# Kernel tuning notes

Hardware: AMD Instinct MI355X
Metric: run time of the kernel (lower is better)

## Reference

```python
import jax, jax.numpy as jnp
import numpy as np

MARGIN = 0.5
EPS = 1e-8  # torch CosineSimilarity eps


def setup_inputs() -> dict:
    key = jax.random.key(0)
    k1, k2 = jax.random.split(key)
    line_end_embeddings = jax.random.normal(k1, (4096, 32, 256), dtype=jnp.float32)
    rhyme_scheme = jax.random.randint(k2, (4096, 32), 0, 4, dtype=jnp.int32)
    return {"line_end_embeddings": line_end_embeddings, "rhyme_scheme": rhyme_scheme}


def reference(line_end_embeddings, rhyme_scheme):
    b, n, d = line_end_embeddings.shape
    # cosine similarity with torch-style eps clamping on norms
    norms = jnp.maximum(jnp.linalg.norm(line_end_embeddings, axis=-1, keepdims=True), EPS)
    unit = line_end_embeddings / norms                       # [b, n, d]
    sims = jnp.einsum("bid,bjd->bij", unit, unit)            # [b, n, n]
    same = rhyme_scheme[:, :, None] == rhyme_scheme[:, None, :]  # [b, n, n]
    per_pair = jnp.where(same, 1.0 - sims, jax.nn.relu(sims - MARGIN))
    # only pairs i < j (strict upper triangle)
    upper = jnp.triu(jnp.ones((n, n), dtype=bool), k=1)
    total = jnp.sum(per_pair * upper[None, :, :])
    count = b * (n * (n - 1) // 2)
    return total / max(count, 1)
```

## Files before the change

kernel.cpp:

```cpp
#include <hip/hip_runtime.h>
#include <hip/hip_bf16.h>


typedef short bf16x8 __attribute__((ext_vector_type(8)));
typedef float f32x4  __attribute__((ext_vector_type(4)));

#define MARGIN 0.5f
#define EPS_NORM 1e-8f
#define NPAIR_INV (1.0f / 2031616.0f)

static __device__ __forceinline__ short f2bf(float f) {
    unsigned u = __float_as_uint(f);
    u += 0x7fffu + ((u >> 16) & 1u);
    return (short)(u >> 16);
}

__global__ __launch_bounds__(256) void rhyme_loss_kernel(
    const float* __restrict__ emb,
    const int*   __restrict__ sch,
    float*       __restrict__ out)
{
    __shared__ float s_diag[4][32];
    __shared__ float s_inv[4][32];
    __shared__ int   s_sch[4][32];

    const int tid  = threadIdx.x;
    const int w    = tid >> 6;
    const int lane = tid & 63;
    const int b    = blockIdx.x * 4 + w;

    const int q = lane >> 4;
    const int c = lane & 15;

    const float* base0 = emb + (size_t)b * 8192 + (size_t)c * 256 + q * 8;
    const float* base1 = base0 + 16 * 256;

    f32x4 acc00 = {0.f, 0.f, 0.f, 0.f};
    f32x4 acc01 = {0.f, 0.f, 0.f, 0.f};
    f32x4 acc11 = {0.f, 0.f, 0.f, 0.f};

    #pragma unroll
    for (int kc = 0; kc < 256; kc += 32) {
        const float4* p0 = (const float4*)(base0 + kc);
        const float4* p1 = (const float4*)(base1 + kc);
        float4 a0 = p0[0], a1 = p0[1];
        float4 b0 = p1[0], b1 = p1[1];

        bf16x8 f0, f1;
        f0[0] = f2bf(a0.x); f0[1] = f2bf(a0.y); f0[2] = f2bf(a0.z); f0[3] = f2bf(a0.w);
        f0[4] = f2bf(a1.x); f0[5] = f2bf(a1.y); f0[6] = f2bf(a1.z); f0[7] = f2bf(a1.w);
        f1[0] = f2bf(b0.x); f1[1] = f2bf(b0.y); f1[2] = f2bf(b0.z); f1[3] = f2bf(b0.w);
        f1[4] = f2bf(b1.x); f1[5] = f2bf(b1.y); f1[6] = f2bf(b1.z); f1[7] = f2bf(b1.w);

        acc00 = __builtin_amdgcn_mfma_f32_16x16x32_bf16(f0, f0, acc00, 0, 0, 0);
        acc01 = __builtin_amdgcn_mfma_f32_16x16x32_bf16(f0, f1, acc01, 0, 0, 0);
        acc11 = __builtin_amdgcn_mfma_f32_16x16x32_bf16(f1, f1, acc11, 0, 0, 0);
    }

    const int dreg = c - 4 * q;
    if (dreg >= 0 && dreg < 4) {
        s_diag[w][c]      = acc00[dreg];
        s_diag[w][16 + c] = acc11[dreg];
    }
    __syncthreads();

    if (lane < 32) {
        float d = s_diag[w][lane];
        s_inv[w][lane] = 1.0f / fmaxf(sqrtf(d), EPS_NORM);
        s_sch[w][lane] = sch[b * 32 + lane];
    }
    __syncthreads();

    const float invj0 = s_inv[w][c];
    const float invj1 = s_inv[w][16 + c];
    const int   sj0   = s_sch[w][c];
    const int   sj1   = s_sch[w][16 + c];

    float sum = 0.0f;
    #pragma unroll
    for (int r = 0; r < 4; ++r) {
        const int   i0    = q * 4 + r;
        const float inv_i = s_inv[w][i0];
        const int   si    = s_sch[w][i0];

        {
            float sim = acc01[r] * inv_i * invj1;
            sum += (si == sj1) ? (1.0f - sim) : fmaxf(sim - MARGIN, 0.0f);
        }
        if (i0 < c) {
            float sim = acc00[r] * inv_i * invj0;
            sum += (si == sj0) ? (1.0f - sim) : fmaxf(sim - MARGIN, 0.0f);
            float sim2 = acc11[r] * s_inv[w][16 + i0] * invj1;
            sum += (s_sch[w][16 + i0] == sj1) ? (1.0f - sim2)
                                              : fmaxf(sim2 - MARGIN, 0.0f);
        }
    }

    #pragma unroll
    for (int off = 32; off > 0; off >>= 1)
        sum += __shfl_down(sum, off, 64);

    if (lane == 0)
        atomicAdd(out, sum * NPAIR_INV);
}

extern "C" void kernel_launch(void* const* d_in, const int* in_sizes, int n_in,
                              void* d_out, int out_size, void* d_ws, size_t ws_size,
                              hipStream_t stream) {
    const float* emb = (const float*)d_in[0];
    const int*   sch = (const int*)d_in[1];
    float*       out = (float*)d_out;

    hipMemsetAsync(out, 0, sizeof(float), stream);
    rhyme_loss_kernel<<<dim3(4096 / 4), dim3(256), 0, stream>>>(emb, sch, out);
}
```

Baseline: 232.9 us.

## Stage embedding rows into LDS via direct global-to-LDS loads, one batch per block

Each batch element's 32x256 fp32 rows are now copied into padded shared memory with global_load_lds, so the global reads are fully coalesced 16-byte-per-lane loads instead of strided per-row float4 loads. The MFMA operands are then read from LDS, with a row stride of 260 to avoid bank conflicts. The launch becomes one 64-thread block per batch, which gives 4x more blocks and one atomic per block. The waitcnt immediate is hard-coded, and each block uses about 33KB of LDS, which limits how many blocks can be resident per CU.

```diff
diff --git a/kernel.cpp b/kernel.cpp
--- a/kernel.cpp
+++ b/kernel.cpp
@@ -1,5 +1,6 @@
 #include <hip/hip_runtime.h>
 #include <hip/hip_bf16.h>
+#include <stdint.h>
 
 
 typedef short bf16x8 __attribute__((ext_vector_type(8)));
@@ -8,6 +9,10 @@
 #define MARGIN 0.5f
 #define EPS_NORM 1e-8f
 #define NPAIR_INV (1.0f / 2031616.0f)
+#define ROW_STRIDE 260
+
+typedef const __attribute__((address_space(1))) void GVOID;
+typedef __attribute__((address_space(3))) void LVOID;
 
 static __device__ __forceinline__ short f2bf(float f) {
     unsigned u = __float_as_uint(f);
@@ -15,25 +20,40 @@
     return (short)(u >> 16);
 }
 
-__global__ __launch_bounds__(256) void rhyme_loss_kernel(
+__global__ __launch_bounds__(64) void rhyme_loss_kernel(
     const float* __restrict__ emb,
     const int*   __restrict__ sch,
     float*       __restrict__ out)
 {
-    __shared__ float s_diag[4][32];
-    __shared__ float s_inv[4][32];
-    __shared__ int   s_sch[4][32];
+    __shared__ float s_rows[32 * ROW_STRIDE];
+    __shared__ float s_inv[32];
+    __shared__ float s_diag[32];
+    __shared__ int   s_sch[32];
 
-    const int tid  = threadIdx.x;
-    const int w    = tid >> 6;
-    const int lane = tid & 63;
-    const int b    = blockIdx.x * 4 + w;
+    const int lane = threadIdx.x;
+    const int b    = blockIdx.x;
 
     const int q = lane >> 4;
     const int c = lane & 15;
 
-    const float* base0 = emb + (size_t)b * 8192 + (size_t)c * 256 + q * 8;
-    const float* base1 = base0 + 16 * 256;
+    const float* gbase = emb + (size_t)b * 8192 + (size_t)lane * 4;
+    #pragma unroll
+    for (int r = 0; r < 32; ++r) {
+        __builtin_amdgcn_global_load_lds(
+            (GVOID*)(gbase + r * 256),
+            (LVOID*)(&s_rows[r * ROW_STRIDE]),
+            16, 0, 0);
+    }
+
+    int mysch = (lane < 32) ? sch[(size_t)b * 32 + lane] : 0;
+
+    __builtin_amdgcn_s_waitcnt(0x0f70);
+    __syncthreads();
+
+    if (lane < 32) s_sch[lane] = mysch;
+
+    const float* r0 = s_rows + (size_t)c * ROW_STRIDE + q * 8;
+    const float* r1 = s_rows + (size_t)(16 + c) * ROW_STRIDE + q * 8;
 
     f32x4 acc00 = {0.f, 0.f, 0.f, 0.f};
     f32x4 acc01 = {0.f, 0.f, 0.f, 0.f};
@@ -41,8 +61,8 @@
 
     #pragma unroll
     for (int kc = 0; kc < 256; kc += 32) {
-        const float4* p0 = (const float4*)(base0 + kc);
-        const float4* p1 = (const float4*)(base1 + kc);
+        const float4* p0 = (const float4*)(r0 + kc);
+        const float4* p1 = (const float4*)(r1 + kc);
         float4 a0 = p0[0], a1 = p0[1];
         float4 b0 = p1[0], b1 = p1[1];
 
@@ -59,29 +79,28 @@
 
     const int dreg = c - 4 * q;
     if (dreg >= 0 && dreg < 4) {
-        s_diag[w][c]      = acc00[dreg];
-        s_diag[w][16 + c] = acc11[dreg];
+        s_diag[c]      = acc00[dreg];
+        s_diag[16 + c] = acc11[dreg];
     }
     __syncthreads();
 
     if (lane < 32) {
-        float d = s_diag[w][lane];
-        s_inv[w][lane] = 1.0f / fmaxf(sqrtf(d), EPS_NORM);
-        s_sch[w][lane] = sch[b * 32 + lane];
+        float d = s_diag[lane];
+        s_inv[lane] = 1.0f / fmaxf(sqrtf(d), EPS_NORM);
     }
     __syncthreads();
 
-    const float invj0 = s_inv[w][c];
-    const float invj1 = s_inv[w][16 + c];
-    const int   sj0   = s_sch[w][c];
-    const int   sj1   = s_sch[w][16 + c];
+    const float invj0 = s_inv[c];
+    const float invj1 = s_inv[16 + c];
+    const int   sj0   = s_sch[c];
+    const int   sj1   = s_sch[16 + c];
 
     float sum = 0.0f;
     #pragma unroll
     for (int r = 0; r < 4; ++r) {
         const int   i0    = q * 4 + r;
-        const float inv_i = s_inv[w][i0];
-        const int   si    = s_sch[w][i0];
+        const float inv_i = s_inv[i0];
+        const int   si    = s_sch[i0];
 
         {
             float sim = acc01[r] * inv_i * invj1;
@@ -90,9 +109,9 @@
         if (i0 < c) {
             float sim = acc00[r] * inv_i * invj0;
             sum += (si == sj0) ? (1.0f - sim) : fmaxf(sim - MARGIN, 0.0f);
-            float sim2 = acc11[r] * s_inv[w][16 + i0] * invj1;
-            sum += (s_sch[w][16 + i0] == sj1) ? (1.0f - sim2)
-                                              : fmaxf(sim2 - MARGIN, 0.0f);
+            float sim2 = acc11[r] * s_inv[16 + i0] * invj1;
+            sum += (s_sch[16 + i0] == sj1) ? (1.0f - sim2)
+                                           : fmaxf(sim2 - MARGIN, 0.0f);
         }
     }
 
@@ -112,5 +131,5 @@
     float*       out = (float*)d_out;
 
     hipMemsetAsync(out, 0, sizeof(float), stream);
-    rhyme_loss_kernel<<<dim3(4096 / 4), dim3(256), 0, stream>>>(emb, sch, out);
+    rhyme_loss_kernel<<<dim3(4096), dim3(64), 0, stream>>>(emb, sch, out);
 }
```

After: 212.0 us. -9.0%, faster.

## Stage embeddings through LDS as bf16 with coalesced block-wide loads

Applied to the files above, without the earlier changes.

Replaces per-lane strided global loads (each lane reading 32 bytes from a different row) with a block-wide coalesced load pass. Each thread reads float4s covering contiguous 4 KB rows, converts them to bf16 and writes them into a padded LDS staging buffer. The MFMA loop then reads bf16x8 fragments from LDS, and scheme values are loaded in the same prologue. This is meant to improve global-memory coalescing and keep more loads in flight, at the cost of about 67 KB of LDS per block, which limits occupancy, plus an extra barrier.

```diff
diff --git a/kernel.cpp b/kernel.cpp
--- a/kernel.cpp
+++ b/kernel.cpp
@@ -1,13 +1,17 @@
 #include <hip/hip_runtime.h>
 #include <hip/hip_bf16.h>
+#include <stdint.h>
 
 
 typedef short bf16x8 __attribute__((ext_vector_type(8)));
+typedef short bf16x4 __attribute__((ext_vector_type(4)));
 typedef float f32x4  __attribute__((ext_vector_type(4)));
 
 #define MARGIN 0.5f
 #define EPS_NORM 1e-8f
 #define NPAIR_INV (1.0f / 2031616.0f)
+#define ROW_S   264
+#define BATCH_S (32 * ROW_S)
 
 static __device__ __forceinline__ short f2bf(float f) {
     unsigned u = __float_as_uint(f);
@@ -20,20 +24,43 @@
     const int*   __restrict__ sch,
     float*       __restrict__ out)
 {
+    __shared__ short s_stage[4 * BATCH_S];
     __shared__ float s_diag[4][32];
     __shared__ float s_inv[4][32];
     __shared__ int   s_sch[4][32];
 
-    const int tid  = threadIdx.x;
-    const int w    = tid >> 6;
-    const int lane = tid & 63;
-    const int b    = blockIdx.x * 4 + w;
+    const int t    = threadIdx.x;
+    const int wv   = t >> 6;
+    const int lane = t & 63;
+
+    const float* gbase = emb + (size_t)blockIdx.x * 32768 + 4 * t;
+
+    if (t < 128)
+        s_sch[t >> 5][t & 31] = sch[(size_t)blockIdx.x * 128 + t];
+
+    #pragma unroll
+    for (int i0 = 0; i0 < 32; i0 += 8) {
+        float4 v[8];
+        #pragma unroll
+        for (int j = 0; j < 8; ++j)
+            v[j] = *(const float4*)(gbase + (size_t)(i0 + j) * 1024);
+        #pragma unroll
+        for (int j = 0; j < 8; ++j) {
+            const int row128 = 4 * (i0 + j) + wv;
+            const int g = row128 >> 5, r = row128 & 31;
+            bf16x4 h;
+            h[0] = f2bf(v[j].x); h[1] = f2bf(v[j].y);
+            h[2] = f2bf(v[j].z); h[3] = f2bf(v[j].w);
+            *(bf16x4*)(&s_stage[g * BATCH_S + r * ROW_S + 4 * lane]) = h;
+        }
+    }
+    __syncthreads();
 
     const int q = lane >> 4;
     const int c = lane & 15;
 
-    const float* base0 = emb + (size_t)b * 8192 + (size_t)c * 256 + q * 8;
-    const float* base1 = base0 + 16 * 256;
+    const short* r0 = s_stage + wv * BATCH_S + c * ROW_S + 8 * q;
+    const short* r1 = s_stage + wv * BATCH_S + (16 + c) * ROW_S + 8 * q;
 
     f32x4 acc00 = {0.f, 0.f, 0.f, 0.f};
     f32x4 acc01 = {0.f, 0.f, 0.f, 0.f};
@@ -41,17 +68,8 @@
 
     #pragma unroll
     for (int kc = 0; kc < 256; kc += 32) {
-        const float4* p0 = (const float4*)(base0 + kc);
-        const float4* p1 = (const float4*)(base1 + kc);
-        float4 a0 = p0[0], a1 = p0[1];
-        float4 b0 = p1[0], b1 = p1[1];
-
-        bf16x8 f0, f1;
-        f0[0] = f2bf(a0.x); f0[1] = f2bf(a0.y); f0[2] = f2bf(a0.z); f0[3] = f2bf(a0.w);
-        f0[4] = f2bf(a1.x); f0[5] = f2bf(a1.y); f0[6] = f2bf(a1.z); f0[7] = f2bf(a1.w);
-        f1[0] = f2bf(b0.x); f1[1] = f2bf(b0.y); f1[2] = f2bf(b0.z); f1[3] = f2bf(b0.w);
-        f1[4] = f2bf(b1.x); f1[5] = f2bf(b1.y); f1[6] = f2bf(b1.z); f1[7] = f2bf(b1.w);
-
+        bf16x8 f0 = *(const bf16x8*)(r0 + kc);
+        bf16x8 f1 = *(const bf16x8*)(r1 + kc);
         acc00 = __builtin_amdgcn_mfma_f32_16x16x32_bf16(f0, f0, acc00, 0, 0, 0);
         acc01 = __builtin_amdgcn_mfma_f32_16x16x32_bf16(f0, f1, acc01, 0, 0, 0);
         acc11 = __builtin_amdgcn_mfma_f32_16x16x32_bf16(f1, f1, acc11, 0, 0, 0);
@@ -59,29 +77,28 @@
 
     const int dreg = c - 4 * q;
     if (dreg >= 0 && dreg < 4) {
-        s_diag[w][c]      = acc00[dreg];
-        s_diag[w][16 + c] = acc11[dreg];
+        s_diag[wv][c]      = acc00[dreg];
+        s_diag[wv][16 + c] = acc11[dreg];
     }
     __syncthreads();
 
     if (lane < 32) {
-        float d = s_diag[w][lane];
-        s_inv[w][lane] = 1.0f / fmaxf(sqrtf(d), EPS_NORM);
-        s_sch[w][lane] = sch[b * 32 + lane];
+        float d = s_diag[wv][lane];
+        s_inv[wv][lane] = 1.0f / fmaxf(sqrtf(d), EPS_NORM);
     }
     __syncthreads();
 
-    const float invj0 = s_inv[w][c];
-    const float invj1 = s_inv[w][16 + c];
-    const int   sj0   = s_sch[w][c];
-    const int   sj1   = s_sch[w][16 + c];
+    const float invj0 = s_inv[wv][c];
+    const float invj1 = s_inv[wv][16 + c];
+    const int   sj0   = s_sch[wv][c];
+    const int   sj1   = s_sch[wv][16 + c];
 
     float sum = 0.0f;
     #pragma unroll
     for (int r = 0; r < 4; ++r) {
         const int   i0    = q * 4 + r;
-        const float inv_i = s_inv[w][i0];
-        const int   si    = s_sch[w][i0];
+        const float inv_i = s_inv[wv][i0];
+        const int   si    = s_sch[wv][i0];
 
         {
             float sim = acc01[r] * inv_i * invj1;
@@ -90,9 +107,9 @@
         if (i0 < c) {
             float sim = acc00[r] * inv_i * invj0;
             sum += (si == sj0) ? (1.0f - sim) : fmaxf(sim - MARGIN, 0.0f);
-            float sim2 = acc11[r] * s_inv[w][16 + i0] * invj1;
-            sum += (s_sch[w][16 + i0] == sj1) ? (1.0f - sim2)
-                                              : fmaxf(sim2 - MARGIN, 0.0f);
+            float sim2 = acc11[r] * s_inv[wv][16 + i0] * invj1;
+            sum += (s_sch[wv][16 + i0] == sj1) ? (1.0f - sim2)
+                                               : fmaxf(sim2 - MARGIN, 0.0f);
         }
     }
 
@@ -112,5 +129,5 @@
     float*       out = (float*)d_out;
 
     hipMemsetAsync(out, 0, sizeof(float), stream);
-    rhyme_loss_kernel<<<dim3(4096 / 4), dim3(256), 0, stream>>>(emb, sch, out);
+    rhyme_loss_kernel<<<dim3(1024), dim3(256), 0, stream>>>(emb, sch, out);
 }
```

After: 223.5 us. -4.1%, faster.

## Split K dimension across wave pairs with LDS reduction of MFMA accumulators

Applied to the files above, without the earlier changes.

Each batch item is now handled by two waves, each covering half of the 256-wide feature dimension, and the partial MFMA accumulators are combined through shared memory. The grid doubles to 2048 blocks of two batch items each, and launch bounds request higher occupancy. The aim is more memory-level parallelism and shorter per-wave dependency chains on a bandwidth-bound kernel, at the cost of an extra LDS exchange, an extra barrier, and half the waves sitting idle during the epilogue.

```diff
diff --git a/kernel.cpp b/kernel.cpp
--- a/kernel.cpp
+++ b/kernel.cpp
@@ -1,5 +1,6 @@
 #include <hip/hip_runtime.h>
 #include <hip/hip_bf16.h>
+#include <stdint.h>
 
 
 typedef short bf16x8 __attribute__((ext_vector_type(8)));
@@ -15,24 +16,30 @@
     return (short)(u >> 16);
 }
 
-__global__ __launch_bounds__(256) void rhyme_loss_kernel(
+__global__ __launch_bounds__(256, 8) void rhyme_loss_kernel(
     const float* __restrict__ emb,
     const int*   __restrict__ sch,
     float*       __restrict__ out)
 {
-    __shared__ float s_diag[4][32];
-    __shared__ float s_inv[4][32];
-    __shared__ int   s_sch[4][32];
+    __shared__ f32x4 s_acc[4][3][64];
+    __shared__ float s_diag[2][32];
+    __shared__ float s_inv[2][32];
+    __shared__ int   s_sch[2][32];
 
-    const int tid  = threadIdx.x;
-    const int w    = tid >> 6;
-    const int lane = tid & 63;
-    const int b    = blockIdx.x * 4 + w;
+    const int t    = threadIdx.x;
+    const int wv   = t >> 6;
+    const int lane = t & 63;
+    const int g    = wv >> 1;
+    const int kh   = wv & 1;
+    const int b    = blockIdx.x * 2 + g;
 
     const int q = lane >> 4;
     const int c = lane & 15;
 
-    const float* base0 = emb + (size_t)b * 8192 + (size_t)c * 256 + q * 8;
+    if (t < 64)
+        s_sch[t >> 5][t & 31] = sch[(size_t)blockIdx.x * 64 + t];
+
+    const float* base0 = emb + (size_t)b * 8192 + (size_t)c * 256 + kh * 128 + q * 8;
     const float* base1 = base0 + 16 * 256;
 
     f32x4 acc00 = {0.f, 0.f, 0.f, 0.f};
@@ -40,11 +47,11 @@
     f32x4 acc11 = {0.f, 0.f, 0.f, 0.f};
 
     #pragma unroll
-    for (int kc = 0; kc < 256; kc += 32) {
-        const float4* p0 = (const float4*)(base0 + kc);
-        const float4* p1 = (const float4*)(base1 + kc);
-        float4 a0 = p0[0], a1 = p0[1];
-        float4 b0 = p1[0], b1 = p1[1];
+    for (int kc = 0; kc < 128; kc += 32) {
+        float4 a0 = *(const float4*)(base0 + kc);
+        float4 a1 = *(const float4*)(base0 + kc + 4);
+        float4 b0 = *(const float4*)(base1 + kc);
+        float4 b1 = *(const float4*)(base1 + kc + 4);
 
         bf16x8 f0, f1;
         f0[0] = f2bf(a0.x); f0[1] = f2bf(a0.y); f0[2] = f2bf(a0.z); f0[3] = f2bf(a0.w);
@@ -57,51 +64,63 @@
         acc11 = __builtin_amdgcn_mfma_f32_16x16x32_bf16(f1, f1, acc11, 0, 0, 0);
     }
 
+    s_acc[wv][0][lane] = acc00;
+    s_acc[wv][1][lane] = acc01;
+    s_acc[wv][2][lane] = acc11;
+    __syncthreads();
+    {
+        const int pw = wv ^ 1;
+        acc00 += s_acc[pw][0][lane];
+        acc01 += s_acc[pw][1][lane];
+        acc11 += s_acc[pw][2][lane];
+    }
+
     const int dreg = c - 4 * q;
-    if (dreg >= 0 && dreg < 4) {
-        s_diag[w][c]      = acc00[dreg];
-        s_diag[w][16 + c] = acc11[dreg];
+    if (kh == 0 && dreg >= 0 && dreg < 4) {
+        s_diag[g][c]      = acc00[dreg];
+        s_diag[g][16 + c] = acc11[dreg];
     }
     __syncthreads();
 
-    if (lane < 32) {
-        float d = s_diag[w][lane];
-        s_inv[w][lane] = 1.0f / fmaxf(sqrtf(d), EPS_NORM);
-        s_sch[w][lane] = sch[b * 32 + lane];
+    if (t < 64) {
+        float d = s_diag[t >> 5][t & 31];
+        s_inv[t >> 5][t & 31] = 1.0f / fmaxf(sqrtf(d), EPS_NORM);
     }
     __syncthreads();
 
-    const float invj0 = s_inv[w][c];
-    const float invj1 = s_inv[w][16 + c];
-    const int   sj0   = s_sch[w][c];
-    const int   sj1   = s_sch[w][16 + c];
+    if (kh == 0) {
+        const float invj0 = s_inv[g][c];
+        const float invj1 = s_inv[g][16 + c];
+        const int   sj0   = s_sch[g][c];
+        const int   sj1   = s_sch[g][16 + c];
 
-    float sum = 0.0f;
-    #pragma unroll
-    for (int r = 0; r < 4; ++r) {
-        const int   i0    = q * 4 + r;
-        const float inv_i = s_inv[w][i0];
-        const int   si    = s_sch[w][i0];
+        float sum = 0.0f;
+        #pragma unroll
+        for (int r = 0; r < 4; ++r) {
+            const int   i0    = q * 4 + r;
+            const float inv_i = s_inv[g][i0];
+            const int   si    = s_sch[g][i0];
 
-        {
-            float sim = acc01[r] * inv_i * invj1;
-            sum += (si == sj1) ? (1.0f - sim) : fmaxf(sim - MARGIN, 0.0f);
+            {
+                float sim = acc01[r] * inv_i * invj1;
+                sum += (si == sj1) ? (1.0f - sim) : fmaxf(sim - MARGIN, 0.0f);
+            }
+            if (i0 < c) {
+                float sim = acc00[r] * inv_i * invj0;
+                sum += (si == sj0) ? (1.0f - sim) : fmaxf(sim - MARGIN, 0.0f);
+                float sim2 = acc11[r] * s_inv[g][16 + i0] * invj1;
+                sum += (s_sch[g][16 + i0] == sj1) ? (1.0f - sim2)
+                                                  : fmaxf(sim2 - MARGIN, 0.0f);
+            }
         }
-        if (i0 < c) {
-            float sim = acc00[r] * inv_i * invj0;
-            sum += (si == sj0) ? (1.0f - sim) : fmaxf(sim - MARGIN, 0.0f);
-            float sim2 = acc11[r] * s_inv[w][16 + i0] * invj1;
-            sum += (s_sch[w][16 + i0] == sj1) ? (1.0f - sim2)
-                                              : fmaxf(sim2 - MARGIN, 0.0f);
-        }
+
+        #pragma unroll
+        for (int off = 32; off > 0; off >>= 1)
+            sum += __shfl_down(sum, off, 64);
+
+        if (lane == 0)
+            atomicAdd(out, sum * NPAIR_INV);
     }
-
-    #pragma unroll
-    for (int off = 32; off > 0; off >>= 1)
-        sum += __shfl_down(sum, off, 64);
-
-    if (lane == 0)
-        atomicAdd(out, sum * NPAIR_INV);
 }
 
 extern "C" void kernel_launch(void* const* d_in, const int* in_sizes, int n_in,
@@ -112,5 +131,5 @@
     float*       out = (float*)d_out;
 
     hipMemsetAsync(out, 0, sizeof(float), stream);
-    rhyme_loss_kernel<<<dim3(4096 / 4), dim3(256), 0, stream>>>(emb, sch, out);
+    rhyme_loss_kernel<<<dim3(2048), dim3(256), 0, stream>>>(emb, sch, out);
 }
```

Result: faster. 215.4 us (-7.5%).
